# Performance work log

Hardware: AMD Instinct MI355X
Metric: run time of the kernel (lower is better)

The kernel has to match this reference:

```python
import jax, jax.numpy as jnp
import numpy as np
import math

B, C, IMG, P = 32, 3, 224, 16
E, DEPTH, H, MLP = 768, 12, 12, 3072
NP = (IMG // P) ** 2          # 196 patches
S = NP + 1                    # 197 tokens with cls
NCLS = 10
HD = E // H                   # 64 head dim
EPS = 1e-5


def setup_inputs() -> dict:
    key = jax.random.key(0)
    ks = iter(jax.random.split(key, 64))
    n = lambda shape, s=0.02: (jax.random.normal(next(ks), shape, jnp.float32) * s)
    inp = {
        "x": jax.random.normal(next(ks), (B, C, IMG, IMG), jnp.float32),
        "conv_w": n((E, C, P, P)),
        "conv_b": jnp.zeros((E,), jnp.float32),
        "cls_token": n((1, 1, E)),
        "pos_embed": n((1, S, E)),
        # stacked per-layer params, leading dim DEPTH; linear weights stored [in, out]
        "ln1_w": jnp.ones((DEPTH, E), jnp.float32),
        "ln1_b": jnp.zeros((DEPTH, E), jnp.float32),
        "qkv_w": n((DEPTH, E, 3 * E)),
        "qkv_b": jnp.zeros((DEPTH, 3 * E), jnp.float32),
        "proj_w": n((DEPTH, E, E)),
        "proj_b": jnp.zeros((DEPTH, E), jnp.float32),
        "ln2_w": jnp.ones((DEPTH, E), jnp.float32),
        "ln2_b": jnp.zeros((DEPTH, E), jnp.float32),
        "mlp_w1": n((DEPTH, E, MLP)),
        "mlp_b1": jnp.zeros((DEPTH, MLP), jnp.float32),
        "mlp_w2": n((DEPTH, MLP, E)),
        "mlp_b2": jnp.zeros((DEPTH, E), jnp.float32),
        "lnf_w": jnp.ones((E,), jnp.float32),
        "lnf_b": jnp.zeros((E,), jnp.float32),
        "head_w": n((E, NCLS)),
        "head_b": jnp.zeros((NCLS,), jnp.float32),
    }
    return inp


def layernorm(x, w, b):
    mu = jnp.mean(x, axis=-1, keepdims=True)
    var = jnp.mean(jnp.square(x - mu), axis=-1, keepdims=True)
    return (x - mu) * jax.lax.rsqrt(var + EPS) * w + b


def reference(x, conv_w, conv_b, cls_token, pos_embed,
              ln1_w, ln1_b, qkv_w, qkv_b, proj_w, proj_b,
              ln2_w, ln2_b, mlp_w1, mlp_b1, mlp_w2, mlp_b2,
              lnf_w, lnf_b, head_w, head_b):
    # --- patch embedding: stride-P, kernel-P conv == patchify + matmul ---
    g = IMG // P  # 14
    patches = x.reshape(B, C, g, P, g, P).transpose(0, 2, 4, 1, 3, 5).reshape(B, NP, C * P * P)
    wp = conv_w.reshape(E, C * P * P)
    tok = jnp.einsum('bpd,ed->bpe', patches, wp) + conv_b  # [B, NP, E]

    # cls token + positional embedding (dropout = identity at eval)
    h = jnp.concatenate([jnp.broadcast_to(cls_token, (B, 1, E)), tok], axis=1) + pos_embed

    scale = math.sqrt(HD)
    for i in range(DEPTH):
        # --- attention ---
        y = layernorm(h, ln1_w[i], ln1_b[i])
        qkv = (y @ qkv_w[i] + qkv_b[i]).reshape(B, S, 3, H, HD)
        q, k, v = qkv[:, :, 0], qkv[:, :, 1], qkv[:, :, 2]  # [B, S, H, HD]
        attn = jnp.einsum('bqhd,bkhd->bhqk', q, k) / scale
        attn = jax.nn.softmax(attn, axis=-1)
        o = jnp.einsum('bhqk,bkhd->bqhd', attn, v).reshape(B, S, E)
        h = h + (o @ proj_w[i] + proj_b[i])
        # --- MLP ---
        y = layernorm(h, ln2_w[i], ln2_b[i])
        y = jax.nn.gelu(y @ mlp_w1[i] + mlp_b1[i], approximate=False)
        h = h + (y @ mlp_w2[i] + mlp_b2[i])

    h = layernorm(h, lnf_w, lnf_b)
    return h[:, 0] @ head_w + head_b  # [B, NCLS]
```

## Files before the change

kernel.cpp:

```cpp
#include <hip/hip_runtime.h>


typedef __attribute__((ext_vector_type(8))) short short8;
typedef __attribute__((ext_vector_type(8))) unsigned short ushort8;
typedef __attribute__((ext_vector_type(4))) float f32x4;
typedef unsigned short u16;

#define DEV __device__ __forceinline__

DEV u16 f2bf(float f) {
  unsigned int u = __builtin_bit_cast(unsigned int, f);
  u += 0x7fffu + ((u >> 16) & 1u);
  return (u16)(u >> 16);
}
DEV float wred_sum(float v) {
  for (int o = 32; o; o >>= 1) v += __shfl_xor(v, o, 64);
  return v;
}
DEV void glds16(const void* gp, void* lp) {
  __builtin_amdgcn_global_load_lds(
      (const __attribute__((address_space(1))) void*)gp,
      (__attribute__((address_space(3))) void*)lp, 16, 0, 0);
}
DEV int xcd_swz(int flat, int nwg) {
  int q = nwg >> 3, r = nwg & 7;
  int x = flat & 7, o = flat >> 3;
  return (x < r ? x * (q + 1) : r * (q + 1) + (x - r) * q) + o;
}

__global__ __launch_bounds__(256) void cvt4_k(const float* __restrict__ s,
                                              u16* __restrict__ d, long n4) {
  long i = (long)blockIdx.x * 256 + threadIdx.x;
  if (i >= n4) return;
  float4 v = ((const float4*)s)[i];
  ushort4 o;
  o.x = f2bf(v.x); o.y = f2bf(v.y); o.z = f2bf(v.z); o.w = f2bf(v.w);
  ((ushort4*)d)[i] = o;
}

__global__ __launch_bounds__(256) void tpose_k(const float* __restrict__ s,
                                               u16* __restrict__ d, int K,
                                               int N) {
  __shared__ float t[32][33];
  const int bx = blockIdx.x;
  const int by = blockIdx.y;
  const size_t base = (size_t)blockIdx.z * K * N;
  const int c = threadIdx.x & 31, r0 = threadIdx.x >> 5;
#pragma unroll
  for (int i = 0; i < 4; ++i) {
    int r = r0 + i * 8;
    t[r][c] = s[base + (size_t)(by * 32 + r) * N + bx * 32 + c];
  }
  __syncthreads();
#pragma unroll
  for (int i = 0; i < 4; ++i) {
    int r = r0 + i * 8;
    d[base + (size_t)(bx * 32 + r) * K + by * 32 + c] = f2bf(t[c][r]);
  }
}

__global__ __launch_bounds__(256) void patch_k(const float* __restrict__ x,
                                               u16* __restrict__ pt) {
  int i = blockIdx.x * 256 + threadIdx.x;
  int d = i % 768;
  int bp = i / 768;
  int p = bp % 196, b = bp / 196;
  int c = d >> 8, pd = d & 255;
  int py = pd >> 4, px = pd & 15;
  int gy = p / 14, gx = p - gy * 14;
  size_t src = ((size_t)(b * 3 + c) * 224 + gy * 16 + py) * 224 + gx * 16 + px;
  pt[i] = f2bf(x[src]);
}

__global__ __launch_bounds__(256) void clspos_k(const float* __restrict__ cls,
                                                const float* __restrict__ pos,
                                                float* __restrict__ h) {
  int i = blockIdx.x * 256 + threadIdx.x;
  int b = i / 768, e = i - b * 768;
  h[(size_t)b * 197 * 768 + e] = cls[e] + pos[e];
}

template <int EPI>
DEV void epi_store(float v, int grow, int gcol, u16* outb, int ldo,
                   float* outf, const float* pos) {
  if constexpr (EPI == 0) {
    outb[(size_t)grow * ldo + gcol] = f2bf(v);
  } else if constexpr (EPI == 1) {
    float u = __expf(-1.5957691216f * (v + 0.044715f * v * v * v));
    outb[(size_t)grow * ldo + gcol] = f2bf(v / (1.f + u));
  } else if constexpr (EPI == 2) {
    outf[(size_t)grow * ldo + gcol] += v;
  } else {
    int b = grow / 196, p = grow - b * 196;
    outf[(size_t)(grow + b + 1) * 768 + gcol] =
        v + pos[(size_t)(p + 1) * 768 + gcol];
  }
}

template <int EPI>
__global__ __launch_bounds__(512) void gemmW2(
    const u16* __restrict__ A, int lda, const u16* __restrict__ Bt, int ldb,
    const float* __restrict__ bias, u16* __restrict__ outb, int ldo,
    float* __restrict__ outf, int M, int K) {
  __shared__ __align__(16) u16 Ak[2][128 * 32];
  __shared__ __align__(16) u16 Bk[2][256 * 32];
  const int tid = threadIdx.x;
  const int lane = tid & 63, wid = tid >> 6;
  const int wm = wid >> 2, wn = wid & 3;
  const int lg = lane >> 4, lr = lane & 15;
  const int nwg = gridDim.x * gridDim.y;
  const int wg = xcd_swz(blockIdx.y * gridDim.x + blockIdx.x, nwg);
  const int tn = wg % gridDim.x, tm = wg / gridDim.x;
  const size_t koff = (EPI == 4) ? (size_t)blockIdx.z * K : 0;

  const int sr = lane >> 2;
  const int sc4 = (((lane & 3) ^ ((lane >> 3) & 3)) << 3);
  const u16* aSrc = A + (size_t)(tm * 128 + wid * 16 + sr) * lda + koff + sc4;
  const u16* bSrc = Bt + (size_t)(tn * 256 + wid * 32 + sr) * ldb + koff + sc4;
  const size_t bRow16 = (size_t)16 * ldb;

  auto stage = [&](int buf, int kt) {
    const u16* ak = aSrc + kt * 32;
    const u16* bk = bSrc + kt * 32;
    glds16(ak, &Ak[buf][wid * 16 * 32]);
    u16* bd = &Bk[buf][wid * 32 * 32];
    glds16(bk, bd);
    glds16(bk + bRow16, bd + 512);
  };

  const int rp = (lg ^ ((lr >> 1) & 3)) << 3;
  f32x4 acc[4][4] = {};
  auto compute = [&](int buf) {
    short8 af[4], bf[4];
#pragma unroll
    for (int i = 0; i < 4; ++i)
      af[i] = *(const short8*)(&Ak[buf][(wm * 64 + i * 16 + lr) * 32 + rp]);
#pragma unroll
    for (int i = 0; i < 4; ++i)
      bf[i] = *(const short8*)(&Bk[buf][(wn * 64 + i * 16 + lr) * 32 + rp]);
#pragma unroll
    for (int mi = 0; mi < 4; ++mi)
#pragma unroll
      for (int ni = 0; ni < 4; ++ni)
        acc[mi][ni] = __builtin_amdgcn_mfma_f32_16x16x32_bf16(
            af[mi], bf[ni], acc[mi][ni], 0, 0, 0);
  };

  const int nk = K >> 5;
  int cur = 0;
  stage(0, 0);
  __syncthreads();
  for (int kt = 0; kt < nk - 1; ++kt) {
    stage(cur ^ 1, kt + 1);
    compute(cur);
    __syncthreads();
    cur ^= 1;
  }
  compute(cur);

#pragma unroll
  for (int mi = 0; mi < 4; ++mi)
#pragma unroll
    for (int ni = 0; ni < 4; ++ni)
#pragma unroll
      for (int r = 0; r < 4; ++r) {
        int grow = tm * 128 + wm * 64 + mi * 16 + lg * 4 + r;
        int gcol = tn * 256 + wn * 64 + ni * 16 + lr;
        if (grow < M) {
          if constexpr (EPI == 4) {
            outf[(size_t)blockIdx.z * M * ldo + (size_t)grow * ldo + gcol] =
                acc[mi][ni][r];
          } else {
            epi_store<EPI>(acc[mi][ni][r] + bias[gcol], grow, gcol, outb, ldo,
                           outf, nullptr);
          }
        }
      }
}

__global__ __launch_bounds__(256) void redK(const float* __restrict__ Cp,
                                            const float* __restrict__ bias,
                                            float* __restrict__ h) {
  size_t i = ((size_t)blockIdx.x * 256 + threadIdx.x) * 4;
  float4 p0 = *(const float4*)(Cp + i);
  float4 p1 = *(const float4*)(Cp + 6304ull * 768 + i);
  float4 p2 = *(const float4*)(Cp + 2ull * 6304 * 768 + i);
  float4 hv = *(const float4*)(h + i);
  float4 bv = *(const float4*)(bias + (int)(i % 768));
  hv.x += p0.x + p1.x + p2.x + bv.x;
  hv.y += p0.y + p1.y + p2.y + bv.y;
  hv.z += p0.z + p1.z + p2.z + bv.z;
  hv.w += p0.w + p1.w + p2.w + bv.w;
  *(float4*)(h + i) = hv;
}

__global__ __launch_bounds__(256) void redln_k(
    const float* __restrict__ Cp, const float* __restrict__ bias,
    float* __restrict__ h, const float* __restrict__ lnw,
    const float* __restrict__ lnb, u16* __restrict__ y) {
  const int lane = threadIdx.x & 63, wv = threadIdx.x >> 6;
  const int r = blockIdx.x * 4 + wv;
  const size_t base = (size_t)r * 768;
  float4 a[3];
  float s = 0.f, q = 0.f;
#pragma unroll
  for (int i = 0; i < 3; ++i) {
    const int off = i * 256 + lane * 4;
    float4 hv = *(const float4*)(h + base + off);
    float4 p0 = *(const float4*)(Cp + base + off);
    float4 p1 = *(const float4*)(Cp + 6304ull * 768 + base + off);
    float4 p2 = *(const float4*)(Cp + 2ull * 6304 * 768 + base + off);
    float4 bv = *(const float4*)(bias + off);
    a[i].x = hv.x + p0.x + p1.x + p2.x + bv.x;
    a[i].y = hv.y + p0.y + p1.y + p2.y + bv.y;
    a[i].z = hv.z + p0.z + p1.z + p2.z + bv.z;
    a[i].w = hv.w + p0.w + p1.w + p2.w + bv.w;
    s += a[i].x + a[i].y + a[i].z + a[i].w;
    q += a[i].x * a[i].x + a[i].y * a[i].y + a[i].z * a[i].z +
         a[i].w * a[i].w;
  }
  s = wred_sum(s);
  q = wred_sum(q);
  float mu = s * (1.f / 768.f);
  float var = q * (1.f / 768.f) - mu * mu;
  float rs = rsqrtf(var + 1e-5f);
#pragma unroll
  for (int i = 0; i < 3; ++i) {
    const int off = i * 256 + lane * 4;
    *(float4*)(h + base + off) = a[i];
    float4 wv4 = *(const float4*)(lnw + off);
    float4 bv4 = *(const float4*)(lnb + off);
    ushort4 o;
    o.x = f2bf((a[i].x - mu) * rs * wv4.x + bv4.x);
    o.y = f2bf((a[i].y - mu) * rs * wv4.y + bv4.y);
    o.z = f2bf((a[i].z - mu) * rs * wv4.z + bv4.z);
    o.w = f2bf((a[i].w - mu) * rs * wv4.w + bv4.w);
    *(ushort4*)(y + base + off) = o;
  }
}

template <int EPI, int BM>
__global__ __launch_bounds__(256) void gemmP(
    const u16* __restrict__ A, int lda, const u16* __restrict__ Bt, int ldb,
    const float* __restrict__ bias, u16* __restrict__ outb, int ldo,
    float* __restrict__ outf, const float* __restrict__ pos, int M, int N,
    int K) {
  constexpr int MI = BM / 32;
  __shared__ __align__(16) u16 Ak[2][BM * 32];
  __shared__ __align__(16) u16 Bk[2][128 * 32];
  const int tid = threadIdx.x;
  const int lane = tid & 63, wid = tid >> 6;
  const int wm = wid >> 1, wn = wid & 1;
  const int lg = lane >> 4, lr = lane & 15;
  const int nwg = gridDim.x * gridDim.y;
  const int wg = xcd_swz(blockIdx.y * gridDim.x + blockIdx.x, nwg);
  const int tn = wg % gridDim.x, tm = wg / gridDim.x;

  const int sr = lane >> 2;
  const int sc4 = (((lane & 3) ^ ((lane >> 3) & 3)) << 3);
  const u16* aSrc = A + (size_t)(tm * BM + wid * (BM / 4) + sr) * lda + sc4;
  const u16* bSrc = Bt + (size_t)(tn * 128 + wid * 32 + sr) * ldb + sc4;
  const size_t aRow16 = (size_t)16 * lda, bRow16 = (size_t)16 * ldb;

  auto stage = [&](int buf, int kt) {
    const u16* ak = aSrc + kt * 32;
    const u16* bk = bSrc + kt * 32;
    u16* ad = &Ak[buf][wid * (BM / 4) * 32];
    u16* bd = &Bk[buf][wid * 1024];
    glds16(ak, ad);
    if constexpr (BM == 128) glds16(ak + aRow16, ad + 512);
    glds16(bk, bd);
    glds16(bk + bRow16, bd + 512);
  };

  const int rp = (lg ^ ((lr >> 1) & 3)) << 3;
  f32x4 acc[MI][4] = {};
  auto compute = [&](int buf) {
    short8 af[MI], bfr[4];
#pragma unroll
    for (int i = 0; i < MI; ++i)
      af[i] =
          *(const short8*)(&Ak[buf][(wm * (BM / 2) + i * 16 + lr) * 32 + rp]);
#pragma unroll
    for (int i = 0; i < 4; ++i)
      bfr[i] = *(const short8*)(&Bk[buf][(wn * 64 + i * 16 + lr) * 32 + rp]);
#pragma unroll
    for (int mi = 0; mi < MI; ++mi)
#pragma unroll
      for (int ni = 0; ni < 4; ++ni)
        acc[mi][ni] = __builtin_amdgcn_mfma_f32_16x16x32_bf16(
            af[mi], bfr[ni], acc[mi][ni], 0, 0, 0);
  };

  const int nk = K >> 5;
  int cur = 0;
  stage(0, 0);
  __syncthreads();
  for (int kt = 0; kt < nk - 1; ++kt) {
    stage(cur ^ 1, kt + 1);
    compute(cur);
    __syncthreads();
    cur ^= 1;
  }
  compute(cur);

#pragma unroll
  for (int mi = 0; mi < MI; ++mi)
#pragma unroll
    for (int ni = 0; ni < 4; ++ni)
#pragma unroll
      for (int r = 0; r < 4; ++r) {
        int grow = tm * BM + wm * (BM / 2) + mi * 16 + lg * 4 + r;
        int gcol = tn * 128 + wn * 64 + ni * 16 + lr;
        if (grow < M)
          epi_store<EPI>(acc[mi][ni][r] + bias[gcol], grow, gcol, outb, ldo,
                         outf, pos);
      }
}

__global__ __launch_bounds__(64) void qksm_k(const u16* __restrict__ qkv,
                                             u16* __restrict__ P) {
  const int bh = blockIdx.x;
  const int qt = blockIdx.y;
  const int lane = threadIdx.x;
  const int lg = lane >> 4, lr = lane & 15;
  const int b = bh / 12, hh = bh - b * 12;
  const u16* base = qkv + (size_t)b * 197 * 2304 + hh * 64;
  int qrow = qt * 16 + lr;
  if (qrow > 196) qrow = 196;
  const u16* qp = base + (size_t)qrow * 2304 + lg * 8;
  short8 a0 = *(const short8*)(qp);
  short8 a1 = *(const short8*)(qp + 32);
  f32x4 c[13];
  const bool kval[2] = {true, (12 * 16 + lr) <= 196};
#pragma unroll
  for (int kt = 0; kt < 13; ++kt) {
    int krow = kt * 16 + lr;
    if (krow > 196) krow = 196;
    const u16* kp = base + 768 + (size_t)krow * 2304 + lg * 8;
    short8 b0 = *(const short8*)(kp);
    short8 b1 = *(const short8*)(kp + 32);
    f32x4 t = {0.f, 0.f, 0.f, 0.f};
    t = __builtin_amdgcn_mfma_f32_16x16x32_bf16(a0, b0, t, 0, 0, 0);
    c[kt] = __builtin_amdgcn_mfma_f32_16x16x32_bf16(a1, b1, t, 0, 0, 0);
  }
  float mr[4], sr_[4];
#pragma unroll
  for (int r = 0; r < 4; ++r) {
    float mm = -3.4e38f;
#pragma unroll
    for (int kt = 0; kt < 13; ++kt)
      if (kval[kt == 12]) mm = fmaxf(mm, c[kt][r] * 0.125f);
#pragma unroll
    for (int o = 1; o < 16; o <<= 1) mm = fmaxf(mm, __shfl_xor(mm, o, 64));
    mr[r] = mm;
  }
#pragma unroll
  for (int r = 0; r < 4; ++r) {
    float s = 0.f;
#pragma unroll
    for (int kt = 0; kt < 13; ++kt) {
      float e = kval[kt == 12] ? __expf(c[kt][r] * 0.125f - mr[r]) : 0.f;
      c[kt][r] = e;
      s += e;
    }
#pragma unroll
    for (int o = 1; o < 16; o <<= 1) s += __shfl_xor(s, o, 64);
    sr_[r] = 1.0f / s;
  }
  u16* pb = P + (size_t)bh * 197 * 224;
#pragma unroll
  for (int r = 0; r < 4; ++r) {
    int q = qt * 16 + lg * 4 + r;
    if (q < 197) {
#pragma unroll
      for (int kt = 0; kt < 13; ++kt)
        pb[(size_t)q * 224 + kt * 16 + lr] = f2bf(c[kt][r] * sr_[r]);
      pb[(size_t)q * 224 + 208 + lr] = 0;
    }
  }
}

__global__ __launch_bounds__(256) void pv_k(const u16* __restrict__ qkv,
                                            const u16* __restrict__ P,
                                            u16* __restrict__ o) {
  __shared__ __align__(16) u16 Vs[224 * 64];
  const int bh = blockIdx.x;
  const int b = bh / 12, hh = bh - b * 12;
  const int tid = threadIdx.x;
  const int lane = tid & 63, ct = tid >> 6;
  const int lg = lane >> 4, lr = lane & 15;
  const u16* vhead = qkv + (size_t)b * 197 * 2304 + 1536 + hh * 64;
#pragma unroll
  for (int it = 0; it < 7; ++it) {
    const int c0 = it * 256 + ct * 64;
    const int c = c0 + lane;
    int row = c >> 3;
    if (row > 196) row = 196;
    glds16(vhead + (size_t)row * 2304 + (c & 7) * 8, &Vs[c0 * 8]);
  }
  __syncthreads();
  short8 vf[7];
#pragma unroll
  for (int ks = 0; ks < 7; ++ks) {
    ushort8 t;
#pragma unroll
    for (int j = 0; j < 8; ++j) {
      int kk = ks * 32 + lg * 8 + j;
      t[j] = Vs[kk * 64 + ct * 16 + lr];
    }
    vf[ks] = __builtin_bit_cast(short8, t);
  }
  const u16* pbase = P + (size_t)bh * 197 * 224;
  u16* ob = o + (size_t)b * 197 * 768 + hh * 64 + ct * 16;
  for (int qt = 0; qt < 13; ++qt) {
    int q = qt * 16 + lr;
    if (q > 196) q = 196;
    const u16* pp = pbase + (size_t)q * 224 + lg * 8;
    f32x4 acc = {0.f, 0.f, 0.f, 0.f};
#pragma unroll
    for (int ks = 0; ks < 7; ++ks) {
      short8 af = *(const short8*)(pp + ks * 32);
      acc = __builtin_amdgcn_mfma_f32_16x16x32_bf16(af, vf[ks], acc, 0, 0, 0);
    }
#pragma unroll
    for (int r = 0; r < 4; ++r) {
      int qq = qt * 16 + lg * 4 + r;
      if (qq < 197) ob[(size_t)qq * 768 + lr] = f2bf(acc[r]);
    }
  }
}

__global__ __launch_bounds__(256) void ln_k(const float* __restrict__ x,
                                            const float* __restrict__ w,
                                            const float* __restrict__ bb,
                                            u16* __restrict__ y) {
  const int lane = threadIdx.x & 63, wv = threadIdx.x >> 6;
  const int r = blockIdx.x * 4 + wv;
  const float* xr = x + (size_t)r * 768;
  float4 v[3];
  float s = 0.f, q = 0.f;
#pragma unroll
  for (int i = 0; i < 3; ++i) {
    v[i] = *(const float4*)(xr + i * 256 + lane * 4);
    s += v[i].x + v[i].y + v[i].z + v[i].w;
    q += v[i].x * v[i].x + v[i].y * v[i].y + v[i].z * v[i].z +
         v[i].w * v[i].w;
  }
  s = wred_sum(s);
  q = wred_sum(q);
  float mu = s * (1.f / 768.f);
  float var = q * (1.f / 768.f) - mu * mu;
  float rs = rsqrtf(var + 1e-5f);
  u16* yr = y + (size_t)r * 768;
#pragma unroll
  for (int i = 0; i < 3; ++i) {
    float4 wv4 = *(const float4*)(w + i * 256 + lane * 4);
    float4 bv4 = *(const float4*)(bb + i * 256 + lane * 4);
    ushort4 o;
    o.x = f2bf((v[i].x - mu) * rs * wv4.x + bv4.x);
    o.y = f2bf((v[i].y - mu) * rs * wv4.y + bv4.y);
    o.z = f2bf((v[i].z - mu) * rs * wv4.z + bv4.z);
    o.w = f2bf((v[i].w - mu) * rs * wv4.w + bv4.w);
    *(ushort4*)(yr + i * 256 + lane * 4) = o;
  }
}

__global__ __launch_bounds__(256) void head_k(
    const float* __restrict__ h, const float* __restrict__ lnw,
    const float* __restrict__ lnb, const float* __restrict__ hw,
    const float* __restrict__ hb, float* __restrict__ out) {
  const int b = blockIdx.x, tid = threadIdx.x;
  const float* xr = h + (size_t)b * 197 * 768;
  float v0 = xr[tid], v1 = xr[tid + 256], v2 = xr[tid + 512];
  float s = v0 + v1 + v2;
  float q = v0 * v0 + v1 * v1 + v2 * v2;
  s = wred_sum(s);
  q = wred_sum(q);
  __shared__ float ss[4], qs[4];
  int lane = tid & 63, wid = tid >> 6;
  if (lane == 0) { ss[wid] = s; qs[wid] = q; }
  __syncthreads();
  float S = ss[0] + ss[1] + ss[2] + ss[3];
  float Q = qs[0] + qs[1] + qs[2] + qs[3];
  float mu = S * (1.f / 768.f);
  float var = Q * (1.f / 768.f) - mu * mu;
  float rs = rsqrtf(var + 1e-5f);
  __shared__ float yb[768];
  yb[tid] = (v0 - mu) * rs * lnw[tid] + lnb[tid];
  yb[tid + 256] = (v1 - mu) * rs * lnw[tid + 256] + lnb[tid + 256];
  yb[tid + 512] = (v2 - mu) * rs * lnw[tid + 512] + lnb[tid + 512];
  __syncthreads();
  float p[10] = {};
  for (int e = tid; e < 768; e += 256) {
    float yv = yb[e];
#pragma unroll
    for (int n = 0; n < 10; ++n) p[n] += yv * hw[(size_t)e * 10 + n];
  }
#pragma unroll
  for (int n = 0; n < 10; ++n) p[n] = wred_sum(p[n]);
  __shared__ float red[4][10];
  if (lane == 0)
#pragma unroll
    for (int n = 0; n < 10; ++n) red[wid][n] = p[n];
  __syncthreads();
  if (tid < 10)
    out[b * 10 + tid] =
        red[0][tid] + red[1][tid] + red[2][tid] + red[3][tid] + hb[tid];
}

extern "C" void kernel_launch(void* const* d_in, const int* in_sizes, int n_in,
                              void* d_out, int out_size, void* d_ws,
                              size_t ws_size, hipStream_t stream) {
  const float* x = (const float*)d_in[0];
  const float* conv_w = (const float*)d_in[1];
  const float* conv_b = (const float*)d_in[2];
  const float* cls = (const float*)d_in[3];
  const float* pos = (const float*)d_in[4];
  const float* ln1w = (const float*)d_in[5];
  const float* ln1b = (const float*)d_in[6];
  const float* qkvw = (const float*)d_in[7];
  const float* qkvbias = (const float*)d_in[8];
  const float* projw = (const float*)d_in[9];
  const float* projb = (const float*)d_in[10];
  const float* ln2w = (const float*)d_in[11];
  const float* ln2b = (const float*)d_in[12];
  const float* w1f = (const float*)d_in[13];
  const float* b1 = (const float*)d_in[14];
  const float* w2f = (const float*)d_in[15];
  const float* b2 = (const float*)d_in[16];
  const float* lnfw = (const float*)d_in[17];
  const float* lnfb = (const float*)d_in[18];
  const float* headw = (const float*)d_in[19];
  const float* headb = (const float*)d_in[20];
  float* out = (float*)d_out;

  char* p = (char*)d_ws;
  auto take = [&](size_t bytes) {
    char* q = p;
    p += (bytes + 255) & ~(size_t)255;
    return q;
  };
  u16* wq = (u16*)take(12ull * 768 * 2304 * 2);
  u16* wpj = (u16*)take(12ull * 768 * 768 * 2);
  u16* w1 = (u16*)take(12ull * 768 * 3072 * 2);
  u16* w2 = (u16*)take(12ull * 3072 * 768 * 2);
  u16* wc = (u16*)take(768ull * 768 * 2);
  float* h = (float*)take(6304ull * 768 * 4);
  u16* y = (u16*)take(6400ull * 768 * 2);
  u16* qkv = (u16*)take(6400ull * 2304 * 2);
  u16* ob = (u16*)take(6400ull * 768 * 2);
  u16* mlpb = (u16*)take(6400ull * 3072 * 2);
  u16* P = (u16*)take(384ull * 197 * 224 * 2);
  float* skP = (float*)take(3ull * 6304 * 768 * 4);
  (void)ws_size; (void)in_sizes; (void)n_in; (void)out_size;

  tpose_k<<<dim3(72, 24, 12), 256, 0, stream>>>(qkvw, wq, 768, 2304);
  tpose_k<<<dim3(24, 24, 12), 256, 0, stream>>>(projw, wpj, 768, 768);
  tpose_k<<<dim3(96, 24, 12), 256, 0, stream>>>(w1f, w1, 768, 3072);
  tpose_k<<<dim3(24, 96, 12), 256, 0, stream>>>(w2f, w2, 3072, 768);
  cvt4_k<<<576, 256, 0, stream>>>(conv_w, wc, 768 * 768 / 4);

  patch_k<<<6272 * 768 / 256, 256, 0, stream>>>(x, mlpb);
  gemmP<3, 64><<<dim3(6, 98), 256, 0, stream>>>(mlpb, 768, wc, 768, conv_b,
                                                nullptr, 0, h, pos, 6272, 768,
                                                768);
  clspos_k<<<32 * 768 / 256, 256, 0, stream>>>(cls, pos, h);

  ln_k<<<1576, 256, 0, stream>>>(h, ln1w, ln1b, y);
  for (int i = 0; i < 12; ++i) {
    gemmW2<0><<<dim3(9, 50), 512, 0, stream>>>(
        y, 768, wq + (size_t)i * 768 * 2304, 768, qkvbias + i * 2304, qkv,
        2304, nullptr, 6304, 768);
    qksm_k<<<dim3(384, 13), 64, 0, stream>>>(qkv, P);
    pv_k<<<384, 256, 0, stream>>>(qkv, P, ob);
    gemmP<2, 64><<<dim3(6, 99), 256, 0, stream>>>(
        ob, 768, wpj + (size_t)i * 768 * 768, 768, projb + i * 768, nullptr,
        768, h, nullptr, 6304, 768, 768);
    ln_k<<<1576, 256, 0, stream>>>(h, ln2w + i * 768, ln2b + i * 768, y);
    gemmW2<1><<<dim3(12, 50), 512, 0, stream>>>(
        y, 768, w1 + (size_t)i * 768 * 3072, 768, b1 + i * 3072, mlpb, 3072,
        nullptr, 6304, 768);
    gemmW2<4><<<dim3(3, 50, 3), 512, 0, stream>>>(
        mlpb, 3072, w2 + (size_t)i * 3072 * 768, 3072, nullptr, nullptr, 768,
        skP, 6304, 1024);
    if (i < 11) {
      redln_k<<<1576, 256, 0, stream>>>(skP, b2 + i * 768, h,
                                        ln1w + (i + 1) * 768,
                                        ln1b + (i + 1) * 768, y);
    } else {
      redK<<<4728, 256, 0, stream>>>(skP, b2 + i * 768, h);
    }
  }

  head_k<<<32, 256, 0, stream>>>(h, lnfw, lnfb, headw, headb, out);
}
```

Before: 3.089 ms.

## Use 128x128 tile with K=64 stage and swizzled LDS for MLP up-projection GEMM

Adds a new GEMM kernel that tiles 128x128 outputs with a 64-deep K stage, XOR-swizzled LDS layout, and double buffering via global_load_lds, then uses it for the MLP fc1+GELU GEMM instead of the 128x256 K=32 kernel. The deeper K step halves the number of barriers per tile, and the swizzle aims to avoid LDS bank conflicts. The smaller N tile doubles the grid to 1200 workgroups, which improves CU fill but lowers reuse of the A operand per block. The last M tile is partial: it stages rows past M from the A buffer, and only the stores are guarded by grow < M.

```diff
diff --git a/kernel.cpp b/kernel.cpp
--- a/kernel.cpp
+++ b/kernel.cpp
@@ -95,6 +95,86 @@
     outf[(size_t)(grow + b + 1) * 768 + gcol] =
         v + pos[(size_t)(p + 1) * 768 + gcol];
   }
+}
+
+template <int EPI>
+__global__ __launch_bounds__(512) void gemmK64(
+    const u16* __restrict__ A, int lda, const u16* __restrict__ Bt, int ldb,
+    const float* __restrict__ bias, u16* __restrict__ outb, int ldo,
+    float* __restrict__ outf, const float* __restrict__ pos, int M, int N,
+    int K) {
+  __shared__ __align__(16) u16 Ak[2][128 * 64];
+  __shared__ __align__(16) u16 Bk[2][128 * 64];
+  const int tid = threadIdx.x;
+  const int lane = tid & 63, wid = tid >> 6;
+  const int wm = wid >> 2, wn = wid & 3;
+  const int lg = lane >> 4, lr = lane & 15;
+  const int nwg = gridDim.x * gridDim.y;
+  const int wg = xcd_swz(blockIdx.y * gridDim.x + blockIdx.x, nwg);
+  const int tn = wg % gridDim.x, tm = wg / gridDim.x;
+
+  const int r8 = lane >> 3, c8 = lane & 7;
+  const int swc = (c8 ^ r8) << 3;
+  const u16* aS = A + (size_t)(tm * 128 + wid * 16 + r8) * lda + swc;
+  const u16* bS = Bt + (size_t)(tn * 128 + wid * 16 + r8) * ldb + swc;
+
+  auto stage = [&](int buf, int kt) {
+    const u16* ak = aS + kt * 64;
+    const u16* bk = bS + kt * 64;
+    u16* ad = &Ak[buf][wid * 1024];
+    u16* bd = &Bk[buf][wid * 1024];
+    glds16(ak, ad);
+    glds16(ak + (size_t)8 * lda, ad + 512);
+    glds16(bk, bd);
+    glds16(bk + (size_t)8 * ldb, bd + 512);
+  };
+
+  f32x4 acc[4][2] = {};
+  auto compute = [&](int buf) {
+#pragma unroll
+    for (int ks = 0; ks < 2; ++ks) {
+      const int pc = (ks << 2) | lg;
+      const int po = ((pc ^ (lr & 7)) << 3);
+      short8 af[4], bf2[2];
+#pragma unroll
+      for (int i = 0; i < 4; ++i)
+        af[i] = *(const short8*)(&Ak[buf][(wm * 64 + i * 16 + lr) * 64 + po]);
+#pragma unroll
+      for (int i = 0; i < 2; ++i)
+        bf2[i] = *(const short8*)(&Bk[buf][(wn * 32 + i * 16 + lr) * 64 + po]);
+#pragma unroll
+      for (int mi = 0; mi < 4; ++mi)
+#pragma unroll
+        for (int ni = 0; ni < 2; ++ni)
+          acc[mi][ni] = __builtin_amdgcn_mfma_f32_16x16x32_bf16(
+              af[mi], bf2[ni], acc[mi][ni], 0, 0, 0);
+    }
+  };
+
+  const int nk = K >> 6;
+  int cur = 0;
+  stage(0, 0);
+  __syncthreads();
+  for (int kt = 0; kt < nk - 1; ++kt) {
+    stage(cur ^ 1, kt + 1);
+    compute(cur);
+    __syncthreads();
+    cur ^= 1;
+  }
+  compute(cur);
+
+#pragma unroll
+  for (int mi = 0; mi < 4; ++mi)
+#pragma unroll
+    for (int ni = 0; ni < 2; ++ni)
+#pragma unroll
+      for (int r = 0; r < 4; ++r) {
+        int grow = tm * 128 + wm * 64 + mi * 16 + lg * 4 + r;
+        int gcol = tn * 128 + wn * 32 + ni * 16 + lr;
+        if (grow < M)
+          epi_store<EPI>(acc[mi][ni][r] + bias[gcol], grow, gcol, outb, ldo,
+                         outf, pos);
+      }
 }
 
 template <int EPI>
@@ -578,9 +658,9 @@
         ob, 768, wpj + (size_t)i * 768 * 768, 768, projb + i * 768, nullptr,
         768, h, nullptr, 6304, 768, 768);
     ln_k<<<1576, 256, 0, stream>>>(h, ln2w + i * 768, ln2b + i * 768, y);
-    gemmW2<1><<<dim3(12, 50), 512, 0, stream>>>(
+    gemmK64<1><<<dim3(24, 50), 512, 0, stream>>>(
         y, 768, w1 + (size_t)i * 768 * 3072, 768, b1 + i * 3072, mlpb, 3072,
-        nullptr, 6304, 768);
+        nullptr, nullptr, 6304, 3072, 768);
     gemmW2<4><<<dim3(3, 50, 3), 512, 0, stream>>>(
         mlpb, 3072, w2 + (size_t)i * 3072 * 768, 3072, nullptr, nullptr, 768,
         skP, 6304, 1024);
```

Result: faster. 2.951 ms (-4.4%).
